# Optimization experiments

Hardware: AMD Instinct MI355X
Metric: run time of the kernel (lower is better)

Reference implementation:

```python
import jax, jax.numpy as jnp
import numpy as np

DIM = 384
HEADS = 12
K = 3          # kernel_size
PAD = 1
STRIDE = 1
B, H, W = 8, 56, 56


def conv1x1(x, w, b=None):
    # x: [B,C,H,W], w: [O,C]
    y = jnp.einsum('bchw,oc->bohw', x, w)
    if b is not None:
        y = y + b[None, :, None, None]
    return y


def unfold(x, k, p, s):
    # torch nn.Unfold: returns patches [B, C, k*k, nH, nW], kernel row-major, channel-major overall
    Bx, C, Hx, Wx = x.shape
    nH = (Hx + 2 * p - k) // s + 1
    nW = (Wx + 2 * p - k) // s + 1
    xp = jnp.pad(x, ((0, 0), (0, 0), (p, p), (p, p)))
    cols = [xp[:, :, i:i + s * nH:s, j:j + s * nW:s] for i in range(k) for j in range(k)]
    return jnp.stack(cols, axis=2), nH, nW


def fold(col, Hx, Wx, k, p, s):
    # torch F.fold (col2im): scatter-add overlapping windows. col: [B, C, k*k, nH, nW]
    Bx, C, _, nH, nW = col.shape
    canvas = jnp.zeros((Bx, C, Hx + 2 * p, Wx + 2 * p), col.dtype)
    idx = 0
    for i in range(k):
        for j in range(k):
            canvas = canvas.at[:, :, i:i + s * nH:s, j:j + s * nW:s].add(col[:, :, idx])
            idx += 1
    return canvas[:, :, p:p + Hx, p:p + Wx]


def setup_inputs() -> dict:
    key = jax.random.key(0)
    ks = jax.random.split(key, 5)
    k2 = K * K
    x = jax.random.normal(ks[0], (B, DIM, H, W), dtype=jnp.float32)
    v_w = jax.random.normal(ks[1], (DIM, DIM), dtype=jnp.float32) * 0.02
    v_b = jnp.zeros((DIM,), dtype=jnp.float32)
    attn_w = jax.random.normal(ks[2], (k2 * k2 * HEADS, DIM), dtype=jnp.float32) * 0.02
    proj_w = jax.random.normal(ks[3], (DIM, DIM), dtype=jnp.float32) * 0.02
    return {'x': x, 'v_w': v_w, 'v_b': v_b, 'attn_w': attn_w, 'proj_w': proj_w}


def reference(x, v_w, v_b, attn_w, proj_w):
    Bx, C, Hx, Wx = x.shape
    k2 = K * K
    hd = C // HEADS  # head dim
    # value projection + unfold into overlapping k x k windows
    v = conv1x1(x, v_w, v_b)
    vcol, nH, nW = unfold(v, K, PAD, STRIDE)        # [B, C, k2, nH, nW]
    L = nH * nW
    v = vcol.reshape(Bx, HEADS, hd, k2, L)          # split C = (heads, hd), heads slow
    v = v.transpose(0, 1, 4, 3, 2)                  # [B, n, L, k2(d), hd]
    # adaptive avg pool to (nH, nW); with stride=1 this is identity (pool window 1)
    ph, pw = Hx // nH, Wx // nW
    xp = x.reshape(Bx, C, nH, ph, nW, pw).mean(axis=(3, 5))
    # per-pixel attention logits, channel layout = ((i*k2 + d)*HEADS + head)
    a = jnp.einsum('bchw,oc->bohw', xp, attn_w)     # [B, k2*k2*n, nH, nW]
    a = a.reshape(Bx, k2, k2, HEADS, L)             # [B, i, d, n, L]
    a = a.transpose(0, 3, 4, 1, 2)                  # [B, n, L, i, d]
    a = jax.nn.softmax(a, axis=-1)
    out = jnp.einsum('bnlid,bnldh->bnlih', a, v)    # [B, n, L, i, hd]
    out = out.transpose(0, 1, 4, 3, 2)              # [B, n, hd, i, L] -> channel (n*hd+h)
    out = out.reshape(Bx, C, k2, nH, nW)
    out = fold(out, Hx, Wx, K, PAD, STRIDE)         # scatter-add windows back
    return conv1x1(out, proj_w)
```

## Files before the change

### kernel.cpp

```cpp
#include <hip/hip_runtime.h>
#include <hip/hip_bf16.h>

#define DIM   384
#define HEADS 12
#define K2    9
#define HH    56
#define WW    56
#define HWP   3136
#define BB    8
#define AO    972
#define AOP   1024
#define PP    3200

typedef __hip_bfloat16 bf16;
typedef short bf16x8 __attribute__((ext_vector_type(8)));
typedef short bf16x4v __attribute__((ext_vector_type(4)));
typedef float f32x4 __attribute__((ext_vector_type(4)));

static __device__ __forceinline__ float b2f(bf16 v) { return __bfloat162float(v); }
static __device__ __forceinline__ float bs2f(short s) {
    return __uint_as_float(((unsigned int)(unsigned short)s) << 16);
}
static __device__ __forceinline__ short f2bs(float f) {
    __hip_bfloat16 h = __float2bfloat16(f);
    return *(short*)&h;
}

static __device__ __forceinline__ void gl_lds16(const bf16* g, bf16* l) {
    __builtin_amdgcn_global_load_lds(
        (const __attribute__((address_space(1))) unsigned int*)g,
        (__attribute__((address_space(3))) unsigned int*)l, 16, 0, 0);
}

__global__ __launch_bounds__(256) void xpose_kernel(
        const float* __restrict__ x, bf16* __restrict__ xT) {
    const int lane = threadIdx.x & 63, w = threadIdx.x >> 6;
    const int p = blockIdx.x * 64 + lane;
    const int b = blockIdx.y;
    bf16* dst = xT + ((size_t)b * PP + p) * DIM;
    if (p >= HWP) {
        bf16x8 z = {};
        for (int cg = w; cg < 48; cg += 4) *(bf16x8*)(dst + cg * 8) = z;
        return;
    }
    const float* src = x + (size_t)b * DIM * HWP + p;
    for (int cg = w; cg < 48; cg += 4) {
        bf16x8 v;
#pragma unroll
        for (int j = 0; j < 8; j++) v[j] = f2bs(src[(size_t)(cg * 8 + j) * HWP]);
        *(bf16x8*)(dst + cg * 8) = v;
    }
}

__global__ __launch_bounds__(256) void wconv_kernel(
        const float* __restrict__ src, bf16* __restrict__ dst, int rows, int rows_pad) {
    int idx = blockIdx.x * 256 + threadIdx.x;
    if (idx >= rows_pad * DIM) return;
    float v = (idx < rows * DIM) ? src[idx] : 0.f;
    *(short*)&dst[idx] = f2bs(v);
}

template<bool OUT_T, bool BIAS, int OSTR, typename TOUT>
__global__ __launch_bounds__(256) void gemm_kernel(
        const bf16* __restrict__ A, const bf16* __restrict__ Bt,
        const float* __restrict__ bias, TOUT* __restrict__ out, int M_out) {
    __shared__ bf16 lds[8192];
    bf16* lA = lds;
    bf16* lB = lds + 4096;
    const int t = threadIdx.x;
    const int lane = t & 63, w = t >> 6;
    const int wm = w & 1, wn = w >> 1;
    const int quad = lane >> 4, l16 = lane & 15;
    const int n0 = blockIdx.x * 128;
    const int m0 = blockIdx.y * 128;
    const int b = blockIdx.z;

    const bf16* Ab = A + (size_t)m0 * DIM;
    const bf16* Bb = Bt + ((size_t)b * PP + n0) * DIM;

    f32x4 acc[4][4] = {};

    for (int k0 = 0; k0 < DIM; k0 += 32) {
#pragma unroll
        for (int r = 0; r < 2; r++) {
            int idx = r * 256 + t;
            gl_lds16(Ab + (size_t)(idx >> 2) * DIM + k0 + (idx & 3) * 8, lA + idx * 8);
        }
#pragma unroll
        for (int r = 0; r < 2; r++) {
            int idx = r * 256 + t;
            gl_lds16(Bb + (size_t)(idx >> 2) * DIM + k0 + (idx & 3) * 8, lB + idx * 8);
        }
        __syncthreads();
        bf16x8 af[4], bfr[4];
#pragma unroll
        for (int mt = 0; mt < 4; mt++)
            af[mt] = *(const bf16x8*)(lA + (wm * 64 + mt * 16 + l16) * 32 + quad * 8);
#pragma unroll
        for (int nt = 0; nt < 4; nt++)
            bfr[nt] = *(const bf16x8*)(lB + (wn * 64 + nt * 16 + l16) * 32 + quad * 8);
#pragma unroll
        for (int mt = 0; mt < 4; mt++)
#pragma unroll
            for (int nt = 0; nt < 4; nt++)
                acc[mt][nt] = __builtin_amdgcn_mfma_f32_16x16x32_bf16(
                    af[mt], bfr[nt], acc[mt][nt], 0, 0, 0);
        __syncthreads();
    }

    if constexpr (!OUT_T) {
#pragma unroll
        for (int mt = 0; mt < 4; mt++) {
#pragma unroll
            for (int nt = 0; nt < 4; nt++) {
                int p = n0 + wn * 64 + nt * 16 + l16;
                if (p >= HWP) continue;
#pragma unroll
                for (int reg = 0; reg < 4; reg++) {
                    int o = m0 + wm * 64 + mt * 16 + quad * 4 + reg;
                    if (o < M_out)
                        out[((size_t)b * M_out + o) * HWP + p] = (TOUT)acc[mt][nt][reg];
                }
            }
        }
    } else {
        bf16* wbuf = lds + w * 1152;
#pragma unroll
        for (int nt = 0; nt < 4; nt++) {
#pragma unroll
            for (int mt = 0; mt < 4; mt++) {
                float4 bi;
                if constexpr (BIAS) bi = *(const float4*)(bias + m0 + wm * 64 + mt * 16 + quad * 4);
                else bi = make_float4(0.f, 0.f, 0.f, 0.f);
                bf16x4v pk;
                pk[0] = f2bs(acc[mt][nt][0] + bi.x);
                pk[1] = f2bs(acc[mt][nt][1] + bi.y);
                pk[2] = f2bs(acc[mt][nt][2] + bi.z);
                pk[3] = f2bs(acc[mt][nt][3] + bi.w);
                *(bf16x4v*)(wbuf + l16 * 72 + mt * 16 + quad * 4) = pk;
            }
            __syncthreads();
            int nr = lane >> 2;
            int mc = (lane & 3) * 16;
            bf16x8 v0 = *(const bf16x8*)(wbuf + nr * 72 + mc);
            bf16x8 v1 = *(const bf16x8*)(wbuf + nr * 72 + mc + 8);
            int p = n0 + wn * 64 + nt * 16 + nr;
            if (p < HWP) {
                bf16* dp = (bf16*)out + ((size_t)b * PP + p) * OSTR + m0 + wm * 64 + mc;
                *(bf16x8*)dp = v0;
                *(bf16x8*)(dp + 8) = v1;
            }
            __syncthreads();
        }
    }
}

__global__ __launch_bounds__(384) void attn_fold_kernel(
        const bf16* __restrict__ lT, const bf16* __restrict__ vT,
        bf16* __restrict__ cT) {
    __shared__ float P[8 * 9 * 12 * 10];
    __shared__ float Wf[8 * 25 * 12];
    const int t = threadIdx.x;
    const int b = blockIdx.y;
    const int pix0 = blockIdx.x * 8;
    const int Y = pix0 / WW, X0 = pix0 % WW;

    for (int r = t; r < 864; r += 384) {
        const int px = r / 108, rem = r % 108;
        const int i = rem / 12, n = rem % 12;
        const int ir = i / 3, ic = i % 3;
        const int yi = Y + 1 - ir, xi = X0 + px + 1 - ic;
        float* Pd = &P[((px * 9 + i) * 12 + n) * 10];
        if (yi < 0 || yi >= HH || xi < 0 || xi >= WW) {
#pragma unroll
            for (int d = 0; d < K2; d++) Pd[d] = 0.f;
        } else {
            const bf16* base = lT + ((size_t)b * PP + yi * WW + xi) * AOP + i * 108 + n;
            float lv[K2];
            float m = -1e30f;
#pragma unroll
            for (int d = 0; d < K2; d++) {
                lv[d] = b2f(base[d * 12]);
                m = fmaxf(m, lv[d]);
            }
            float s = 0.f;
#pragma unroll
            for (int d = 0; d < K2; d++) { lv[d] = __expf(lv[d] - m); s += lv[d]; }
            const float inv = 1.f / s;
#pragma unroll
            for (int d = 0; d < K2; d++) Pd[d] = lv[d] * inv;
        }
    }
    __syncthreads();

    for (int e = t; e < 2400; e += 384) {
        const int px = e / 300, rem = e % 300;
        const int off = rem / 12, n = rem % 12;
        const int dy = off / 5 - 2, dx = off % 5 - 2;
        const int ir_lo = max(0, -dy), ir_hi = min(2, 2 - dy);
        const int ic_lo = max(0, -dx), ic_hi = min(2, 2 - dx);
        float wsum = 0.f;
        for (int ir = ir_lo; ir <= ir_hi; ir++)
            for (int ic = ic_lo; ic <= ic_hi; ic++) {
                const int i = ir * 3 + ic;
                const int d = (dy + ir) * 3 + (dx + ic);
                wsum += P[((px * 9 + i) * 12 + n) * 10 + d];
            }
        Wf[e] = wsum;
    }
    __syncthreads();

    const int px = t / 48, cg = t % 48;
    const int X = X0 + px;
    const int n = cg >> 2;
    const float* Wp = &Wf[px * 300];
    const bf16* vb = vT + (size_t)b * PP * DIM;
    float acc[8] = {};
#pragma unroll
    for (int dy = -2; dy <= 2; dy++) {
        const int ny = Y + dy;
        if (ny < 0 || ny >= HH) continue;
#pragma unroll
        for (int dx = -2; dx <= 2; dx++) {
            const int nx = X + dx;
            const bool ok = (nx >= 0 && nx < WW);
            const int nxc = min(max(nx, 0), WW - 1);
            const float w = ok ? Wp[((dy + 2) * 5 + dx + 2) * 12 + n] : 0.f;
            bf16x8 vv = *(const bf16x8*)(vb + (size_t)(ny * WW + nxc) * DIM + cg * 8);
#pragma unroll
            for (int j = 0; j < 8; j++) acc[j] += w * bs2f(vv[j]);
        }
    }
    bf16x8 po;
#pragma unroll
    for (int j = 0; j < 8; j++) po[j] = f2bs(acc[j]);
    *(bf16x8*)(cT + ((size_t)b * PP + pix0 + px) * DIM + cg * 8) = po;
}

extern "C" void kernel_launch(void* const* d_in, const int* in_sizes, int n_in,
                              void* d_out, int out_size, void* d_ws, size_t ws_size,
                              hipStream_t stream) {
    const float* x      = (const float*)d_in[0];
    const float* v_w    = (const float*)d_in[1];
    const float* v_b    = (const float*)d_in[2];
    const float* attn_w = (const float*)d_in[3];
    const float* proj_w = (const float*)d_in[4];
    float* out = (float*)d_out;

    bf16* xT   = (bf16*)d_ws;
    bf16* vT   = xT + (size_t)BB * PP * DIM;
    bf16* lT   = vT + (size_t)BB * PP * DIM;
    bf16* wv   = lT + (size_t)BB * PP * AOP;
    bf16* wa   = wv + 384 * DIM;
    bf16* wp   = wa + AOP * DIM;
    bf16* cT   = xT;

    wconv_kernel<<<(384 * DIM + 255) / 256, 256, 0, stream>>>(v_w, wv, 384, 384);
    wconv_kernel<<<(AOP * DIM + 255) / 256, 256, 0, stream>>>(attn_w, wa, AO, AOP);
    wconv_kernel<<<(384 * DIM + 255) / 256, 256, 0, stream>>>(proj_w, wp, 384, 384);
    xpose_kernel<<<dim3(PP / 64, BB), 256, 0, stream>>>(x, xT);

    gemm_kernel<true, true, DIM, bf16><<<dim3(PP / 128, 3, BB), 256, 0, stream>>>(wv, xT, v_b, vT, DIM);
    gemm_kernel<true, false, AOP, bf16><<<dim3(PP / 128, AOP / 128, BB), 256, 0, stream>>>(wa, xT, nullptr, lT, AOP);
    attn_fold_kernel<<<dim3(HWP / 8, BB), 384, 0, stream>>>(lT, vT, cT);
    gemm_kernel<false, false, 0, float><<<dim3(PP / 128, 3, BB), 256, 0, stream>>>(wp, cT, nullptr, out, DIM);
}
```

Measured before the change: 253.3 us.

## Merge value and logit GEMMs; stage attention logits in LDS with coalesced loads

Concatenates the value and attention-logit weight matrices so one GEMM launch produces both vT and lT. Each block routes its output tile to the right buffer and applies the bias only on the value part. The attention-fold kernel now cooperatively loads the needed logit rows into shared memory with vectorized loads, instead of strided scalar global reads per softmax. Softmax then reads from LDS, and the LDS buffer is reused for the fold weights. This removes a kernel launch and the scattered global reads of logits, at the cost of recomputing softmax for overlapping neighbour pixels (90 combos vs 72) and a more complex index mapping.

After: 314.3 us. 24.1% more time.

```diff
diff --git a/kernel.cpp b/kernel.cpp
--- a/kernel.cpp
+++ b/kernel.cpp
@@ -10,6 +10,7 @@
 #define BB    8
 #define AO    972
 #define AOP   1024
+#define MCAT  1408
 #define PP    3200
 
 typedef __hip_bfloat16 bf16;
@@ -60,10 +61,41 @@
     *(short*)&dst[idx] = f2bs(v);
 }
 
-template<bool OUT_T, bool BIAS, int OSTR, typename TOUT>
-__global__ __launch_bounds__(256) void gemm_kernel(
+#define GEMM_MAIN_LOOP(Ab, Bb, lA, lB, acc)                                    \
+    for (int k0 = 0; k0 < DIM; k0 += 32) {                                     \
+        _Pragma("unroll")                                                      \
+        for (int r = 0; r < 2; r++) {                                          \
+            int idx = r * 256 + t;                                             \
+            gl_lds16(Ab + (size_t)(idx >> 2) * DIM + k0 + (idx & 3) * 8,       \
+                     lA + idx * 8);                                            \
+        }                                                                      \
+        _Pragma("unroll")                                                      \
+        for (int r = 0; r < 2; r++) {                                          \
+            int idx = r * 256 + t;                                             \
+            gl_lds16(Bb + (size_t)(idx >> 2) * DIM + k0 + (idx & 3) * 8,       \
+                     lB + idx * 8);                                            \
+        }                                                                      \
+        __syncthreads();                                                       \
+        bf16x8 af[4], bfr[4];                                                  \
+        _Pragma("unroll")                                                      \
+        for (int mt = 0; mt < 4; mt++)                                         \
+            af[mt] = *(const bf16x8*)(lA + (wm * 64 + mt * 16 + l16) * 32 + quad * 8); \
+        _Pragma("unroll")                                                      \
+        for (int nt = 0; nt < 4; nt++)                                         \
+            bfr[nt] = *(const bf16x8*)(lB + (wn * 64 + nt * 16 + l16) * 32 + quad * 8); \
+        _Pragma("unroll")                                                      \
+        for (int mt = 0; mt < 4; mt++)                                         \
+            _Pragma("unroll")                                                  \
+            for (int nt = 0; nt < 4; nt++)                                     \
+                acc[mt][nt] = __builtin_amdgcn_mfma_f32_16x16x32_bf16(         \
+                    af[mt], bfr[nt], acc[mt][nt], 0, 0, 0);                    \
+        __syncthreads();                                                       \
+    }
+
+__global__ __launch_bounds__(256) void gemm12_kernel(
         const bf16* __restrict__ A, const bf16* __restrict__ Bt,
-        const float* __restrict__ bias, TOUT* __restrict__ out, int M_out) {
+        const float* __restrict__ bias, bf16* __restrict__ vT,
+        bf16* __restrict__ lT) {
     __shared__ bf16 lds[8192];
     bf16* lA = lds;
     bf16* lB = lds + 4096;
@@ -79,78 +111,73 @@
     const bf16* Bb = Bt + ((size_t)b * PP + n0) * DIM;
 
     f32x4 acc[4][4] = {};
-
-    for (int k0 = 0; k0 < DIM; k0 += 32) {
-#pragma unroll
-        for (int r = 0; r < 2; r++) {
-            int idx = r * 256 + t;
-            gl_lds16(Ab + (size_t)(idx >> 2) * DIM + k0 + (idx & 3) * 8, lA + idx * 8);
-        }
-#pragma unroll
-        for (int r = 0; r < 2; r++) {
-            int idx = r * 256 + t;
-            gl_lds16(Bb + (size_t)(idx >> 2) * DIM + k0 + (idx & 3) * 8, lB + idx * 8);
+    GEMM_MAIN_LOOP(Ab, Bb, lA, lB, acc)
+
+    const bool isv = (m0 < 384);
+    bf16* outp = isv ? vT : lT;
+    const int ostr = isv ? DIM : AOP;
+    const int ch0 = isv ? m0 : m0 - 384;
+
+    bf16* wbuf = lds + w * 1152;
+#pragma unroll
+    for (int nt = 0; nt < 4; nt++) {
+#pragma unroll
+        for (int mt = 0; mt < 4; mt++) {
+            float4 bi = make_float4(0.f, 0.f, 0.f, 0.f);
+            if (isv) bi = *(const float4*)(bias + ch0 + wm * 64 + mt * 16 + quad * 4);
+            bf16x4v pk;
+            pk[0] = f2bs(acc[mt][nt][0] + bi.x);
+            pk[1] = f2bs(acc[mt][nt][1] + bi.y);
+            pk[2] = f2bs(acc[mt][nt][2] + bi.z);
+            pk[3] = f2bs(acc[mt][nt][3] + bi.w);
+            *(bf16x4v*)(wbuf + l16 * 72 + mt * 16 + quad * 4) = pk;
         }
         __syncthreads();
-        bf16x8 af[4], bfr[4];
-#pragma unroll
-        for (int mt = 0; mt < 4; mt++)
-            af[mt] = *(const bf16x8*)(lA + (wm * 64 + mt * 16 + l16) * 32 + quad * 8);
-#pragma unroll
-        for (int nt = 0; nt < 4; nt++)
-            bfr[nt] = *(const bf16x8*)(lB + (wn * 64 + nt * 16 + l16) * 32 + quad * 8);
-#pragma unroll
-        for (int mt = 0; mt < 4; mt++)
-#pragma unroll
-            for (int nt = 0; nt < 4; nt++)
-                acc[mt][nt] = __builtin_amdgcn_mfma_f32_16x16x32_bf16(
-                    af[mt], bfr[nt], acc[mt][nt], 0, 0, 0);
+        int nr = lane >> 2;
+        int mc = (lane & 3) * 16;
+        bf16x8 v0 = *(const bf16x8*)(wbuf + nr * 72 + mc);
+        bf16x8 v1 = *(const bf16x8*)(wbuf + nr * 72 + mc + 8);
+        int p = n0 + wn * 64 + nt * 16 + nr;
+        if (p < HWP) {
+            bf16* dp = outp + ((size_t)b * PP + p) * ostr + ch0 + wm * 64 + mc;
+            *(bf16x8*)dp = v0;
+            *(bf16x8*)(dp + 8) = v1;
+        }
         __syncthreads();
     }
-
-    if constexpr (!OUT_T) {
-#pragma unroll
-        for (int mt = 0; mt < 4; mt++) {
-#pragma unroll
-            for (int nt = 0; nt < 4; nt++) {
-                int p = n0 + wn * 64 + nt * 16 + l16;
-                if (p >= HWP) continue;
-#pragma unroll
-                for (int reg = 0; reg < 4; reg++) {
-                    int o = m0 + wm * 64 + mt * 16 + quad * 4 + reg;
-                    if (o < M_out)
-                        out[((size_t)b * M_out + o) * HWP + p] = (TOUT)acc[mt][nt][reg];
-                }
+}
+
+__global__ __launch_bounds__(256) void gemm_planar_kernel(
+        const bf16* __restrict__ A, const bf16* __restrict__ Bt,
+        float* __restrict__ out) {
+    __shared__ bf16 lds[8192];
+    bf16* lA = lds;
+    bf16* lB = lds + 4096;
+    const int t = threadIdx.x;
+    const int lane = t & 63, w = t >> 6;
+    const int wm = w & 1, wn = w >> 1;
+    const int quad = lane >> 4, l16 = lane & 15;
+    const int n0 = blockIdx.x * 128;
+    const int m0 = blockIdx.y * 128;
+    const int b = blockIdx.z;
+
+    const bf16* Ab = A + (size_t)m0 * DIM;
+    const bf16* Bb = Bt + ((size_t)b * PP + n0) * DIM;
+
+    f32x4 acc[4][4] = {};
+    GEMM_MAIN_LOOP(Ab, Bb, lA, lB, acc)
+
+#pragma unroll
+    for (int mt = 0; mt < 4; mt++) {
+#pragma unroll
+        for (int nt = 0; nt < 4; nt++) {
+            int p = n0 + wn * 64 + nt * 16 + l16;
+            if (p >= HWP) continue;
+#pragma unroll
+            for (int reg = 0; reg < 4; reg++) {
+                int o = m0 + wm * 64 + mt * 16 + quad * 4 + reg;
+                out[((size_t)b * DIM + o) * HWP + p] = acc[mt][nt][reg];
             }
-        }
-    } else {
-        bf16* wbuf = lds + w * 1152;
-#pragma unroll
-        for (int nt = 0; nt < 4; nt++) {
-#pragma unroll
-            for (int mt = 0; mt < 4; mt++) {
-                float4 bi;
-                if constexpr (BIAS) bi = *(const float4*)(bias + m0 + wm * 64 + mt * 16 + quad * 4);
-                else bi = make_float4(0.f, 0.f, 0.f, 0.f);
-                bf16x4v pk;
-                pk[0] = f2bs(acc[mt][nt][0] + bi.x);
-                pk[1] = f2bs(acc[mt][nt][1] + bi.y);
-                pk[2] = f2bs(acc[mt][nt][2] + bi.z);
-                pk[3] = f2bs(acc[mt][nt][3] + bi.w);
-                *(bf16x4v*)(wbuf + l16 * 72 + mt * 16 + quad * 4) = pk;
-            }
-            __syncthreads();
-            int nr = lane >> 2;
-            int mc = (lane & 3) * 16;
-            bf16x8 v0 = *(const bf16x8*)(wbuf + nr * 72 + mc);
-            bf16x8 v1 = *(const bf16x8*)(wbuf + nr * 72 + mc + 8);
-            int p = n0 + wn * 64 + nt * 16 + nr;
-            if (p < HWP) {
-                bf16* dp = (bf16*)out + ((size_t)b * PP + p) * OSTR + m0 + wm * 64 + mc;
-                *(bf16x8*)dp = v0;
-                *(bf16x8*)(dp + 8) = v1;
-            }
-            __syncthreads();
         }
     }
 }
@@ -158,29 +185,42 @@
 __global__ __launch_bounds__(384) void attn_fold_kernel(
         const bf16* __restrict__ lT, const bf16* __restrict__ vT,
         bf16* __restrict__ cT) {
-    __shared__ float P[8 * 9 * 12 * 10];
-    __shared__ float Wf[8 * 25 * 12];
+    __shared__ float P[90 * 12 * 9];
+    __shared__ __align__(16) char U[30 * 328 * 2];
+    bf16* L = (bf16*)U;
+    float* Wf = (float*)U;
     const int t = threadIdx.x;
     const int b = blockIdx.y;
     const int pix0 = blockIdx.x * 8;
     const int Y = pix0 / WW, X0 = pix0 % WW;
 
-    for (int r = t; r < 864; r += 384) {
-        const int px = r / 108, rem = r % 108;
-        const int i = rem / 12, n = rem % 12;
-        const int ir = i / 3, ic = i % 3;
-        const int yi = Y + 1 - ir, xi = X0 + px + 1 - ic;
-        float* Pd = &P[((px * 9 + i) * 12 + n) * 10];
+    for (int task = t; task < 2430; task += 384) {
+        const int combo = task / 81, j = task % 81;
+        const int ir = combo / 10, xoff = combo % 10;
+        const int yi = Y + 1 - ir, xi = X0 - 1 + xoff;
+        if (yi >= 0 && yi < HH && xi >= 0 && xi < WW) {
+            const bf16* src = lT + ((size_t)(b * PP) + yi * WW + xi) * AOP + ir * 324 + j * 4;
+            *(bf16x4v*)(L + combo * 328 + j * 4) = *(const bf16x4v*)src;
+        }
+    }
+    __syncthreads();
+
+    for (int sm = t; sm < 1080; sm += 384) {
+        const int slice = sm / 12, n = sm % 12;
+        const int combo = slice / 3, ic = slice % 3;
+        const int ir = combo / 10, xoff = combo % 10;
+        const int yi = Y + 1 - ir, xi = X0 - 1 + xoff;
+        float* Pd = &P[sm * 9];
         if (yi < 0 || yi >= HH || xi < 0 || xi >= WW) {
 #pragma unroll
             for (int d = 0; d < K2; d++) Pd[d] = 0.f;
         } else {
-            const bf16* base = lT + ((size_t)b * PP + yi * WW + xi) * AOP + i * 108 + n;
+            const bf16* Lb = L + combo * 328 + ic * 108 + n;
             float lv[K2];
             float m = -1e30f;
 #pragma unroll
             for (int d = 0; d < K2; d++) {
-                lv[d] = b2f(base[d * 12]);
+                lv[d] = b2f(Lb[d * 12]);
                 m = fmaxf(m, lv[d]);
             }
             float s = 0.f;
@@ -202,9 +242,9 @@
         float wsum = 0.f;
         for (int ir = ir_lo; ir <= ir_hi; ir++)
             for (int ic = ic_lo; ic <= ic_hi; ic++) {
-                const int i = ir * 3 + ic;
+                const int slice = (ir * 10 + (px + 2 - ic)) * 3 + ic;
                 const int d = (dy + ir) * 3 + (dx + ic);
-                wsum += P[((px * 9 + i) * 12 + n) * 10 + d];
+                wsum += P[(slice * 12 + n) * 9 + d];
             }
         Wf[e] = wsum;
     }
@@ -247,21 +287,19 @@
     const float* proj_w = (const float*)d_in[4];
     float* out = (float*)d_out;
 
-    bf16* xT   = (bf16*)d_ws;
-    bf16* vT   = xT + (size_t)BB * PP * DIM;
-    bf16* lT   = vT + (size_t)BB * PP * DIM;
-    bf16* wv   = lT + (size_t)BB * PP * AOP;
-    bf16* wa   = wv + 384 * DIM;
-    bf16* wp   = wa + AOP * DIM;
-    bf16* cT   = xT;
-
-    wconv_kernel<<<(384 * DIM + 255) / 256, 256, 0, stream>>>(v_w, wv, 384, 384);
-    wconv_kernel<<<(AOP * DIM + 255) / 256, 256, 0, stream>>>(attn_w, wa, AO, AOP);
+    bf16* xT    = (bf16*)d_ws;
+    bf16* vT    = xT + (size_t)BB * PP * DIM;
+    bf16* lT    = vT + (size_t)BB * PP * DIM;
+    bf16* wcat  = lT + (size_t)BB * PP * AOP;
+    bf16* wp    = wcat + (size_t)MCAT * DIM;
+    bf16* cT    = xT;
+
+    wconv_kernel<<<(384 * DIM + 255) / 256, 256, 0, stream>>>(v_w, wcat, 384, 384);
+    wconv_kernel<<<(1024 * DIM + 255) / 256, 256, 0, stream>>>(attn_w, wcat + 384 * DIM, AO, 1024);
     wconv_kernel<<<(384 * DIM + 255) / 256, 256, 0, stream>>>(proj_w, wp, 384, 384);
     xpose_kernel<<<dim3(PP / 64, BB), 256, 0, stream>>>(x, xT);
 
-    gemm_kernel<true, true, DIM, bf16><<<dim3(PP / 128, 3, BB), 256, 0, stream>>>(wv, xT, v_b, vT, DIM);
-    gemm_kernel<true, false, AOP, bf16><<<dim3(PP / 128, AOP / 128, BB), 256, 0, stream>>>(wa, xT, nullptr, lT, AOP);
+    gemm12_kernel<<<dim3(PP / 128, MCAT / 128, BB), 256, 0, stream>>>(wcat, xT, v_b, vT, lT);
     attn_fold_kernel<<<dim3(HWP / 8, BB), 384, 0, stream>>>(lT, vT, cT);
-    gemm_kernel<false, false, 0, float><<<dim3(PP / 128, 3, BB), 256, 0, stream>>>(wp, cT, nullptr, out, DIM);
-}
+    gemm_planar_kernel<<<dim3(PP / 128, 3, BB), 256, 0, stream>>>(wp, cT, out);
+}
```
